# Kernel optimization log

Hardware: AMD Instinct MI355X
Metric: run time of the kernel (lower is better)

Reference implementation:

```python
import jax, jax.numpy as jnp
from jax import lax
import numpy as np

N_QUBITS = 8
Q_DEPTH = 10
DIM = 256  # 2**8

# basis-state bit table; wire 0 = most-significant bit (PennyLane convention)
_bits = ((np.arange(DIM)[:, None] >> (N_QUBITS - 1 - np.arange(N_QUBITS))) & 1)
# phase layer: S on even wires (phase i), T on odd wires (phase e^{i pi/4})
_ph = np.where(np.arange(N_QUBITS) % 2 == 0, 1j, np.exp(1j * np.pi / 4))
_diag = np.prod(np.power(_ph[None, :], _bits), axis=1)
# entangling_layer_3 CZ pattern
_cz = np.ones(DIM)
for i, j in [(0, 1), (2, 3), (4, 5), (6, 7), (1, 2), (3, 4), (5, 6)]:
    _cz = _cz * ((-1.0) ** (_bits[:, i] * _bits[:, j]))
DIAG = jnp.asarray((_diag * _cz).astype(np.complex64))  # phase+CZ layer fused diagonal
ZSIGNS = jnp.asarray((1 - 2 * _bits).astype(np.float32))  # [256, 8] PauliZ eigenvalues
H_GATE = jnp.asarray((np.array([[1.0, 1.0], [1.0, -1.0]]) / np.sqrt(2.0)).astype(np.complex64))
X_GATE = jnp.asarray(np.array([[0.0, 1.0], [1.0, 0.0]]).astype(np.complex64))
EYE2 = jnp.eye(2, dtype=jnp.complex64)
BN_EPS = 1e-5


def apply_1q(state, U, w):
    """Apply 2x2 gate U on wire w; state: [B, 2,2,...,2]."""
    state = jnp.moveaxis(state, w + 1, -1)
    state = jnp.matmul(state, U.T)
    return jnp.moveaxis(state, -1, w + 1)


def quantum_net(features, q_params):
    """Batched statevector sim of quantum_net_3. features [B,256], q_params [80] -> [B,8]."""
    f = features / jnp.linalg.norm(features, axis=1, keepdims=True)
    state = f.astype(jnp.complex64).reshape((-1,) + (2,) * N_QUBITS)
    for w in range(N_QUBITS):
        state = apply_1q(state, H_GATE, w)
    qw = q_params.reshape(Q_DEPTH, N_QUBITS)
    for layer in range(Q_DEPTH):
        for w in range(N_QUBITS):
            t = qw[layer, w]
            c = jnp.cos(t / 2).astype(jnp.complex64)
            s = jnp.sin(t / 2).astype(jnp.complex64)
            U = c * EYE2 + (-1j) * s * X_GATE  # RX(t)
            state = apply_1q(state, U, w)
        flat = state.reshape(-1, DIM) * DIAG  # phase layer + CZ entangling (diagonal)
        state = flat.reshape((-1,) + (2,) * N_QUBITS)
    sv = state.reshape(-1, DIM)
    probs = sv.real ** 2 + sv.imag ** 2
    return probs @ ZSIGNS  # [B, 8] expval(PauliZ_i)


def conv2d(x, w, b):
    y = lax.conv_general_dilated(x, w, (1, 1), 'SAME', dimension_numbers=('NCHW', 'OIHW', 'NCHW'))
    return y + b[None, :, None, None]


def bn(x, gamma, beta, mean, var):  # eval-mode BatchNorm2d
    inv = gamma / jnp.sqrt(var + BN_EPS)
    return x * inv[None, :, None, None] + (beta - mean * inv)[None, :, None, None]


def maxpool2(x):
    return lax.reduce_window(x, -jnp.inf, lax.max, (1, 1, 2, 2), (1, 1, 2, 2), 'VALID')


def setup_inputs() -> dict:
    key = jax.random.key(0)
    ks = jax.random.split(key, 16)
    B = 1024
    return {
        'x': jax.random.normal(ks[0], (B, 1, 28, 28), dtype=jnp.float32),
        'conv1_w': 0.1 * jax.random.normal(ks[1], (32, 1, 3, 3), dtype=jnp.float32),
        'conv1_b': jnp.zeros((32,), jnp.float32),
        'bn1_gamma': jnp.ones((32,), jnp.float32),
        'bn1_beta': jnp.zeros((32,), jnp.float32),
        'bn1_mean': jnp.zeros((32,), jnp.float32),
        'bn1_var': jnp.ones((32,), jnp.float32),
        'conv2_w': 0.05 * jax.random.normal(ks[2], (64, 32, 3, 3), dtype=jnp.float32),
        'conv2_b': jnp.zeros((64,), jnp.float32),
        'bn2_gamma': jnp.ones((64,), jnp.float32),
        'bn2_beta': jnp.zeros((64,), jnp.float32),
        'bn2_mean': jnp.zeros((64,), jnp.float32),
        'bn2_var': jnp.ones((64,), jnp.float32),
        'fc_w': 0.01 * jax.random.normal(ks[3], (256, 64 * 7 * 7), dtype=jnp.float32),
        'fc_b': jnp.zeros((256,), jnp.float32),
        'q_params': 0.1 * jax.random.normal(ks[4], (Q_DEPTH * N_QUBITS,), dtype=jnp.float32),
        'p1_w': 0.01 * jax.random.normal(ks[5], (128, 8), dtype=jnp.float32),
        'p1_b': jnp.zeros((128,), jnp.float32),
        'p2_w': 0.01 * jax.random.normal(ks[6], (64, 128), dtype=jnp.float32),
        'p2_b': jnp.zeros((64,), jnp.float32),
        'p3_w': 0.01 * jax.random.normal(ks[7], (10, 64), dtype=jnp.float32),
        'p3_b': jnp.zeros((10,), jnp.float32),
    }


def reference(x, conv1_w, conv1_b, bn1_gamma, bn1_beta, bn1_mean, bn1_var,
              conv2_w, conv2_b, bn2_gamma, bn2_beta, bn2_mean, bn2_var,
              fc_w, fc_b, q_params, p1_w, p1_b, p2_w, p2_b, p3_w, p3_b):
    h = maxpool2(jax.nn.relu(bn(conv2d(x, conv1_w, conv1_b), bn1_gamma, bn1_beta, bn1_mean, bn1_var)))
    h = maxpool2(jax.nn.relu(bn(conv2d(h, conv2_w, conv2_b), bn2_gamma, bn2_beta, bn2_mean, bn2_var)))
    h = h.reshape(h.shape[0], -1)  # [B, 64*7*7]
    feats = jnp.tanh(h @ fc_w.T + fc_b)  # [B, 256]
    q = quantum_net(feats, q_params)  # [B, 8]
    z = jax.nn.relu(q @ p1_w.T + p1_b)  # dropout = identity (eval)
    z = jax.nn.relu(z @ p2_w.T + p2_b)
    return z @ p3_w.T + p3_b
```

## Files before the change

### kernel.cpp

```cpp
#include <hip/hip_runtime.h>
#include <math.h>


#define B_SZ 1024

#define OFF_FCWP   0
#define OFF_W2F    802816
#define OFF_SC2    821600
#define OFF_SH2    821664
#define OFF_H1     821728
#define OFF_H2P    7244256

#define KSPLIT_FC 14
#define TS 40

typedef __attribute__((ext_vector_type(8))) short s16x8;
typedef __attribute__((ext_vector_type(4))) float f32x4;

__constant__ float C_COS8[8] = {1.f, 0.70710678f, 0.f, -0.70710678f, -1.f, -0.70710678f, 0.f, 0.70710678f};
__constant__ float C_SIN8[8] = {0.f, 0.70710678f, 1.f, 0.70710678f, 0.f, -0.70710678f, -1.f, -0.70710678f};

__device__ __forceinline__ unsigned short bf16_rne(float f) {
  unsigned u = __float_as_uint(f);
  unsigned r = u + 0x7FFFu + ((u >> 16) & 1u);
  return (unsigned short)(r >> 16);
}
__device__ __forceinline__ int div14(int m) {
  return __float2int_rz((float)m * 0.07142858f);
}

__global__ __launch_bounds__(256) void fused_front_kernel(
    const float* __restrict__ x, const float* __restrict__ c1w, const float* __restrict__ c1b,
    const float* __restrict__ bn1g, const float* __restrict__ bn1b, const float* __restrict__ bn1m,
    const float* __restrict__ bn1v,
    const float* __restrict__ c2w,
    const float* __restrict__ bn2g, const float* __restrict__ bn2b, const float* __restrict__ bn2m,
    const float* __restrict__ bn2v, const float* __restrict__ c2b,
    const float* __restrict__ fc_w,
    float* __restrict__ ws) {
  const int blk = blockIdx.x, tid = threadIdx.x;
  __shared__ float smem[3136];

  if (blk >= 1024) {
    if (blk < 1280) {
      const int n = blk - 1024;
      const float* src = fc_w + n * 3136;
      for (int i = tid; i < 3136; i += 256) smem[i] = src[i];
      __syncthreads();
      unsigned short* us = (unsigned short*)ws;
      const int nt = n >> 4, nl = n & 15;
      for (int idx = tid; idx < 784; idx += 256) {
        const int part = (idx >= 392);
        const int rest = idx - part * 392;
        const int kg = rest >> 2, q = rest & 3;
        s16x8 v;
#pragma unroll
        for (int j = 0; j < 8; ++j) {
          const int k = kg * 32 + q * 8 + j;
          float f = smem[(k & 63) * 49 + (k >> 6)];
          unsigned short hi = bf16_rne(f);
          unsigned short r = hi;
          if (part) r = bf16_rne(f - __uint_as_float((unsigned)hi << 16));
          v[j] = (short)r;
        }
        *(s16x8*)&us[((((kg * 16 + nt) * 2 + part)) << 9) + (q * 16 + nl) * 8] = v;
      }
    } else if (blk < 1424) {
      int g = (blk - 1280) * 256 + tid;
      int j = g & 7, L = (g >> 3) & 63, rest = g >> 9;
      int h = rest & 1; rest >>= 1;
      int t = rest % 9, w = rest / 9;
      int occ = w * 16 + (L & 15);
      int ic  = (L >> 4) * 8 + j;
      float v = c2w[occ * 288 + ic * 9 + t];
      unsigned short hi = bf16_rne(v);
      unsigned short res = hi;
      if (h) res = bf16_rne(v - __uint_as_float((unsigned)hi << 16));
      ((unsigned short*)(ws + OFF_W2F))[g] = res;
    } else {
      if (tid < 64) {
        float inv = bn2g[tid] / sqrtf(bn2v[tid] + 1e-5f);
        ws[OFF_SC2 + tid] = inv;
        ws[OFF_SH2 + tid] = c2b[tid] * inv + bn2b[tid] - bn2m[tid] * inv;
      }
    }
    return;
  }

  const int b = blk;
  float (*xs)[32] = (float (*)[32])smem;
  float* w1s  = smem + 960;
  float* sc1s = smem + 1248;
  float* sh1s = smem + 1280;
  float* h1 = ws + OFF_H1;

  if (tid < 240) ((float4*)smem)[tid] = make_float4(0.f, 0.f, 0.f, 0.f);
  __syncthreads();
  const float* xb = x + b * 784;
  for (int i = tid; i < 784; i += 256) {
    int y = i / 28, c = i - y * 28;
    xs[y + 1][c + 1] = xb[i];
  }
  for (int i = tid; i < 288; i += 256) w1s[i] = c1w[(i & 31) * 9 + (i >> 5)];
  if (tid < 32) {
    float inv = bn1g[tid] / sqrtf(bn1v[tid] + 1e-5f);
    sc1s[tid] = inv;
    sh1s[tid] = c1b[tid] * inv + bn1b[tid] - bn1m[tid] * inv;
  }
  __syncthreads();

  for (int t = tid; t < 448; t += 256) {
    const int oc = t & 31, py = t >> 5;
    float wv[9];
#pragma unroll
    for (int k = 0; k < 9; ++k) wv[k] = w1s[k * 32 + oc];
    float acc0[28], acc1[28];
#pragma unroll
    for (int j = 0; j < 28; ++j) { acc0[j] = 0.f; acc1[j] = 0.f; }
#pragma unroll
    for (int r = 0; r < 4; ++r) {
      const int pr = 2 * py + r;
      float row[32];
#pragma unroll
      for (int q = 0; q < 8; ++q) {
        float4 v = *(const float4*)&xs[pr][4 * q];
        row[4 * q] = v.x; row[4 * q + 1] = v.y; row[4 * q + 2] = v.z; row[4 * q + 3] = v.w;
      }
      if (r <= 2) {
#pragma unroll
        for (int kx = 0; kx < 3; ++kx) {
          const float w = wv[r * 3 + kx];
#pragma unroll
          for (int xx = 0; xx < 28; ++xx) acc0[xx] = fmaf(row[xx + kx], w, acc0[xx]);
        }
      }
      if (r >= 1) {
#pragma unroll
        for (int kx = 0; kx < 3; ++kx) {
          const float w = wv[(r - 1) * 3 + kx];
#pragma unroll
          for (int xx = 0; xx < 28; ++xx) acc1[xx] = fmaf(row[xx + kx], w, acc1[xx]);
        }
      }
    }
    const float sc = sc1s[oc], sh = sh1s[oc];
    float* dst = h1 + b * 6272 + oc * 196 + py * 14;
#pragma unroll
    for (int px = 0; px < 14; ++px) {
      float v0 = fmaxf(fmaf(acc0[2 * px], sc, sh), 0.f);
      float v1 = fmaxf(fmaf(acc0[2 * px + 1], sc, sh), 0.f);
      float v2 = fmaxf(fmaf(acc1[2 * px], sc, sh), 0.f);
      float v3 = fmaxf(fmaf(acc1[2 * px + 1], sc, sh), 0.f);
      dst[px] = fmaxf(fmaxf(v0, v1), fmaxf(v2, v3));
    }
  }
}

__global__ __launch_bounds__(256, 2) void conv2_kernel(
    const float* __restrict__ h1, const float* __restrict__ w2f_f,
    const float* __restrict__ sc2, const float* __restrict__ sh2,
    unsigned short* __restrict__ h2hi, unsigned short* __restrict__ h2lo) {
  const int b = blockIdx.x, tid = threadIdx.x;
  const int lane = tid & 63, w = tid >> 6;
  const int mh = w >> 1, nh = w & 1;

  __shared__ unsigned char lds_raw[50176];
  unsigned short* tile_hi = (unsigned short*)lds_raw;
  unsigned short* tile_lo = (unsigned short*)(lds_raw + 21760);
  float* conv_out = (float*)lds_raw;

  const unsigned short* w2f = (const unsigned short*)w2f_f;
  s16x8 bf[9][2][2];
#pragma unroll
  for (int t = 0; t < 9; ++t)
#pragma unroll
    for (int ntl = 0; ntl < 2; ++ntl)
#pragma unroll
      for (int h = 0; h < 2; ++h)
        bf[t][ntl][h] = *(const s16x8*)&w2f[(((((nh * 2 + ntl) * 9 + t) * 2 + h)) << 9) + lane * 8];

  {
    float4* z = (float4*)lds_raw;
    for (int i = tid; i < 2720; i += 256) z[i] = make_float4(0.f, 0.f, 0.f, 0.f);
  }
  __syncthreads();

  if (tid < 196) {
    const int y = div14(tid), x = tid - y * 14;
    const int sp = ((y + 1) * 16 + (x + 1)) * TS;
    const float* src = h1 + b * 6272 + tid;
#pragma unroll
    for (int c = 0; c < 4; ++c) {
      s16x8 hv, lv;
#pragma unroll
      for (int j = 0; j < 8; ++j) {
        float v = src[(c * 8 + j) * 196];
        unsigned short h16 = bf16_rne(v);
        hv[j] = (short)h16;
        lv[j] = (short)bf16_rne(v - __uint_as_float((unsigned)h16 << 16));
      }
      *(s16x8*)&tile_hi[sp + c * 8] = hv;
      *(s16x8*)&tile_lo[sp + c * 8] = lv;
    }
  }
  __syncthreads();

  const int nmt = 7 - mh;
  const int mt0 = mh * 7;
  f32x4 acc[7][2];
#pragma unroll
  for (int i = 0; i < 7; ++i) { acc[i][0] = (f32x4){0,0,0,0}; acc[i][1] = (f32x4){0,0,0,0}; }

  const int kg8 = (lane >> 4) * 8;
#pragma unroll
  for (int mi = 0; mi < 7; ++mi) {
    if (mi < nmt) {
      const int m = (mt0 + mi) * 16 + (lane & 15);
      const int y = div14(m), x = m - y * 14;
      const int base = (y * 16 + x) * TS + kg8;
#pragma unroll
      for (int dy = 0; dy < 3; ++dy) {
#pragma unroll
        for (int dx = 0; dx < 3; ++dx) {
          const int off = base + (dy * 16 + dx) * TS;
          s16x8 ah = *(s16x8*)&tile_hi[off];
          s16x8 al = *(s16x8*)&tile_lo[off];
          const int t = dy * 3 + dx;
#pragma unroll
          for (int ntl = 0; ntl < 2; ++ntl) {
            acc[mi][ntl] = __builtin_amdgcn_mfma_f32_16x16x32_bf16(ah, bf[t][ntl][0], acc[mi][ntl], 0, 0, 0);
            acc[mi][ntl] = __builtin_amdgcn_mfma_f32_16x16x32_bf16(ah, bf[t][ntl][1], acc[mi][ntl], 0, 0, 0);
            acc[mi][ntl] = __builtin_amdgcn_mfma_f32_16x16x32_bf16(al, bf[t][ntl][0], acc[mi][ntl], 0, 0, 0);
          }
        }
      }
    }
  }
  __syncthreads();

#pragma unroll
  for (int mi = 0; mi < 7; ++mi) {
    if (mi < nmt) {
#pragma unroll
      for (int ntl = 0; ntl < 2; ++ntl) {
        const int oc = nh * 32 + ntl * 16 + (lane & 15);
        const float sc = sc2[oc], sh = sh2[oc];
#pragma unroll
        for (int r = 0; r < 4; ++r) {
          const int m = (mt0 + mi) * 16 + (lane >> 4) * 4 + r;
          if (m < 196) conv_out[m * 64 + oc] = fmaxf(fmaf(acc[mi][ntl][r], sc, sh), 0.f);
        }
      }
    }
  }
  __syncthreads();

  const int oc = tid & 63;
#pragma unroll
  for (int i = 0; i < 13; ++i) {
    const int ps = i * 4 + (tid >> 6);
    if (ps < 49) {
      const int py = (ps * 37) >> 8, px = ps - py * 7;
      const int m00 = py * 28 + px * 2;
      float v0 = conv_out[m00 * 64 + oc];
      float v1 = conv_out[(m00 + 1) * 64 + oc];
      float v2 = conv_out[(m00 + 14) * 64 + oc];
      float v3 = conv_out[(m00 + 15) * 64 + oc];
      float vm = fmaxf(fmaxf(v0, v1), fmaxf(v2, v3));
      unsigned short hv = bf16_rne(vm);
      const int idx = b * 3136 + ps * 64 + oc;
      h2hi[idx] = hv;
      h2lo[idx] = bf16_rne(vm - __uint_as_float((unsigned)hv << 16));
    }
  }
}

__global__ __launch_bounds__(256) void fc_mfma_kernel(
    const unsigned short* __restrict__ h2hi, const unsigned short* __restrict__ h2lo,
    const unsigned short* __restrict__ Bfrag, float* __restrict__ Part) {
  const int tid = threadIdx.x;
  const int lane = tid & 63, w = tid >> 6;
  const int nt0 = blockIdx.x * 4, z = blockIdx.z;
  const int mrow = blockIdx.y * 64 + w * 16 + (lane & 15);
  const int kg8 = (lane >> 4) * 8;
  const unsigned short* arow_hi = h2hi + mrow * 3136 + kg8;
  const unsigned short* arow_lo = h2lo + mrow * 3136 + kg8;

  f32x4 acc[4];
#pragma unroll
  for (int i = 0; i < 4; ++i) acc[i] = (f32x4){0.f, 0.f, 0.f, 0.f};

#pragma unroll
  for (int c = 0; c < 7; ++c) {
    const int kg = z * 7 + c;
    s16x8 ah = *(const s16x8*)(arow_hi + kg * 32);
    s16x8 al = *(const s16x8*)(arow_lo + kg * 32);
#pragma unroll
    for (int nf = 0; nf < 4; ++nf) {
      const unsigned short* bp = Bfrag + (size_t)((kg * 16 + nt0 + nf) * 2) * 512 + lane * 8;
      s16x8 bh = *(const s16x8*)bp;
      s16x8 bl = *(const s16x8*)(bp + 512);
      acc[nf] = __builtin_amdgcn_mfma_f32_16x16x32_bf16(ah, bh, acc[nf], 0, 0, 0);
      acc[nf] = __builtin_amdgcn_mfma_f32_16x16x32_bf16(ah, bl, acc[nf], 0, 0, 0);
      acc[nf] = __builtin_amdgcn_mfma_f32_16x16x32_bf16(al, bh, acc[nf], 0, 0, 0);
    }
  }

  float* dst = Part + (size_t)z * 262144;
  const int mbase = blockIdx.y * 64 + w * 16 + (lane >> 4) * 4;
  const int nbase = (lane & 15);
#pragma unroll
  for (int nf = 0; nf < 4; ++nf) {
#pragma unroll
    for (int r = 0; r < 4; ++r) {
      dst[(mbase + r) * 256 + (nt0 + nf) * 16 + nbase] = acc[nf][r];
    }
  }
}

__global__ __launch_bounds__(64) void quantum_kernel(
    const float* __restrict__ Part, const float* __restrict__ fc_b,
    const float* __restrict__ qp,
    const float* __restrict__ p1w, const float* __restrict__ p1b,
    const float* __restrict__ p2w, const float* __restrict__ p2b,
    const float* __restrict__ p3w, const float* __restrict__ p3b,
    float* __restrict__ out) {
  const int b = blockIdx.x, lane = threadIdx.x;
  __shared__ float csl[160];

  for (int g = lane; g < 80; g += 64) {
    float t = 0.5f * qp[g];
    csl[2 * g] = cosf(t);
    csl[2 * g + 1] = sinf(t);
  }
  __syncthreads();

  float fa[4];
#pragma unroll
  for (int a = 0; a < 4; ++a) {
    const int idx = a * 64 + lane;
    float f = fc_b[idx];
#pragma unroll
    for (int z = 0; z < KSPLIT_FC; ++z) f += Part[z * 262144 + b * 256 + idx];
    fa[a] = tanhf(f);
  }
  float ss = fa[0] * fa[0] + fa[1] * fa[1] + fa[2] * fa[2] + fa[3] * fa[3];
#pragma unroll
  for (int off = 32; off >= 1; off >>= 1) ss += __shfl_xor(ss, off);
  const float inv = 1.0f / sqrtf(ss);

  float re[4], im[4];
#pragma unroll
  for (int a = 0; a < 4; ++a) { re[a] = fa[a] * inv; im[a] = 0.f; }

  float dre[4], dim_[4];
#pragma unroll
  for (int a = 0; a < 4; ++a) {
    const int i = a * 64 + lane;
    const int k8 = (2 * __popc(i & 0xAA) + __popc(i & 0x55)) & 7;
    float dr = C_COS8[k8], di = C_SIN8[k8];
    int par = ((i >> 7) & (i >> 6)) ^ ((i >> 5) & (i >> 4)) ^ ((i >> 3) & (i >> 2)) ^ ((i >> 1) & i)
            ^ ((i >> 6) & (i >> 5)) ^ ((i >> 4) & (i >> 3)) ^ ((i >> 2) & (i >> 1));
    if (par & 1) { dr = -dr; di = -di; }
    dre[a] = dr; dim_[a] = di;
  }

  const float RS = 0.70710678118654752f;

#define H_PAIR(u, v)                                        \
  { float tur = re[u], tui = im[u];                         \
    re[u] = (tur + re[v]) * RS; im[u] = (tui + im[v]) * RS; \
    re[v] = (tur - re[v]) * RS; im[v] = (tui - im[v]) * RS; }
  H_PAIR(0, 2) H_PAIR(1, 3)
  H_PAIR(0, 1) H_PAIR(2, 3)
#pragma unroll
  for (int w = 2; w < 8; ++w) {
    const int m = 1 << (7 - w);
    const float sgn = (lane & m) ? -1.f : 1.f;
#pragma unroll
    for (int a = 0; a < 4; ++a) {
      float pre = __shfl_xor(re[a], m);
      float pim = __shfl_xor(im[a], m);
      re[a] = fmaf(sgn, re[a], pre) * RS;
      im[a] = fmaf(sgn, im[a], pim) * RS;
    }
  }

#define RX_PAIR(u, v, c, s)                                   \
  { float ur = re[u], ui = im[u], wr = re[v], wi = im[v];     \
    re[u] = fmaf(s, wi, c * ur); im[u] = fmaf(-s, wr, c * ui);\
    re[v] = fmaf(s, ui, c * wr); im[v] = fmaf(-s, ur, c * wi); }
  for (int layer = 0; layer < 10; ++layer) {
    const float* cs = &csl[16 * layer];
    { const float c = cs[0], s = cs[1]; RX_PAIR(0, 2, c, s) RX_PAIR(1, 3, c, s) }
    { const float c = cs[2], s = cs[3]; RX_PAIR(0, 1, c, s) RX_PAIR(2, 3, c, s) }
#pragma unroll
    for (int w = 2; w < 8; ++w) {
      const int m = 1 << (7 - w);
      const float c = cs[2 * w], s = cs[2 * w + 1];
#pragma unroll
      for (int a = 0; a < 4; ++a) {
        float pre = __shfl_xor(re[a], m);
        float pim = __shfl_xor(im[a], m);
        float nre = fmaf(s, pim, c * re[a]);
        float nim = fmaf(-s, pre, c * im[a]);
        if (w == 7) {
          float tre = nre * dre[a] - nim * dim_[a];
          nim = fmaf(nre, dim_[a], nim * dre[a]);
          nre = tre;
        }
        re[a] = nre; im[a] = nim;
      }
    }
  }

  float prb[4];
#pragma unroll
  for (int a = 0; a < 4; ++a) prb[a] = re[a] * re[a] + im[a] * im[a];
  float qv[8];
#pragma unroll
  for (int w = 0; w < 8; ++w) {
    float v;
    if (w == 0)      v = prb[0] + prb[1] - prb[2] - prb[3];
    else if (w == 1) v = prb[0] - prb[1] + prb[2] - prb[3];
    else {
      const int m = 1 << (7 - w);
      const float sgn = (lane & m) ? -1.f : 1.f;
      v = sgn * (prb[0] + prb[1] + prb[2] + prb[3]);
    }
#pragma unroll
    for (int off = 32; off >= 1; off >>= 1) v += __shfl_xor(v, off);
    qv[w] = v;
  }

  float z1a = p1b[lane], z1b = p1b[lane + 64];
#pragma unroll
  for (int k = 0; k < 8; ++k) {
    z1a = fmaf(qv[k], p1w[lane * 8 + k], z1a);
    z1b = fmaf(qv[k], p1w[(lane + 64) * 8 + k], z1b);
  }
  z1a = fmaxf(z1a, 0.f); z1b = fmaxf(z1b, 0.f);

  float acc2 = p2b[lane];
  const float* row2 = p2w + lane * 128;
#pragma unroll
  for (int kc = 0; kc < 64; kc += 4) {
    float4 w0 = *(const float4*)&row2[kc];
    float4 w1 = *(const float4*)&row2[64 + kc];
    float wv0[4] = {w0.x, w0.y, w0.z, w0.w};
    float wv1[4] = {w1.x, w1.y, w1.z, w1.w};
#pragma unroll
    for (int j = 0; j < 4; ++j) {
      acc2 = fmaf(__shfl(z1a, kc + j), wv0[j], acc2);
      acc2 = fmaf(__shfl(z1b, kc + j), wv1[j], acc2);
    }
  }
  const float z2 = fmaxf(acc2, 0.f);

#pragma unroll
  for (int n = 0; n < 10; ++n) {
    float p = z2 * p3w[n * 64 + lane];
#pragma unroll
    for (int off = 32; off >= 1; off >>= 1) p += __shfl_xor(p, off);
    if (lane == n) out[b * 10 + n] = p + p3b[n];
  }
}

extern "C" void kernel_launch(void* const* d_in, const int* in_sizes, int n_in,
                              void* d_out, int out_size, void* d_ws, size_t ws_size,
                              hipStream_t stream) {
  (void)in_sizes; (void)n_in; (void)out_size; (void)ws_size;
  const float* x    = (const float*)d_in[0];
  const float* c1w  = (const float*)d_in[1];
  const float* c1b  = (const float*)d_in[2];
  const float* bn1g = (const float*)d_in[3];
  const float* bn1b = (const float*)d_in[4];
  const float* bn1m = (const float*)d_in[5];
  const float* bn1v = (const float*)d_in[6];
  const float* c2w  = (const float*)d_in[7];
  const float* c2b  = (const float*)d_in[8];
  const float* bn2g = (const float*)d_in[9];
  const float* bn2b = (const float*)d_in[10];
  const float* bn2m = (const float*)d_in[11];
  const float* bn2v = (const float*)d_in[12];
  const float* fc_w = (const float*)d_in[13];
  const float* fc_b = (const float*)d_in[14];
  const float* qp   = (const float*)d_in[15];
  const float* p1w  = (const float*)d_in[16];
  const float* p1b  = (const float*)d_in[17];
  const float* p2w  = (const float*)d_in[18];
  const float* p2b  = (const float*)d_in[19];
  const float* p3w  = (const float*)d_in[20];
  const float* p3b  = (const float*)d_in[21];
  float* ws = (float*)d_ws;
  float* outp = (float*)d_out;

  unsigned short* h2hi = (unsigned short*)(ws + OFF_H2P);
  unsigned short* h2lo = h2hi + 3211264;
  const unsigned short* bfrag = (const unsigned short*)ws;

  fused_front_kernel<<<1425, 256, 0, stream>>>(x, c1w, c1b, bn1g, bn1b, bn1m, bn1v,
                                               c2w, bn2g, bn2b, bn2m, bn2v, c2b, fc_w, ws);
  conv2_kernel<<<B_SZ, 256, 0, stream>>>(ws + OFF_H1, ws + OFF_W2F, ws + OFF_SC2, ws + OFF_SH2,
                                         h2hi, h2lo);
  fc_mfma_kernel<<<dim3(4, 16, KSPLIT_FC), 256, 0, stream>>>(h2hi, h2lo, bfrag, ws + OFF_H1);
  quantum_kernel<<<B_SZ, 64, 0, stream>>>(ws + OFF_H1, fc_b, qp, p1w, p1b, p2w, p2b, p3w, p3b, outp);
}
```

Baseline: 179.5 us.

## Fuse conv1 into conv2 kernel, writing pooled activations straight to LDS tiles

Conv1+BN+ReLU+maxpool now runs inside the conv2 block and writes its bf16 hi/lo split directly into the shared-memory input tiles. This removes the global round trip of the h1 intermediate (about 25 MB written and read back) and one kernel boundary. Weight packing moves to a separate small prep kernel that runs first. The cost is that the scalar conv1 phase now runs in a block using about 49KB of LDS and the register-resident weight fragments. That can lower occupancy for the conv1 part and serialise it before the MFMA work in the same block.

```diff
diff --git a/kernel.cpp b/kernel.cpp
--- a/kernel.cpp
+++ b/kernel.cpp
@@ -29,73 +29,93 @@
   return __float2int_rz((float)m * 0.07142858f);
 }
 
-__global__ __launch_bounds__(256) void fused_front_kernel(
+__global__ __launch_bounds__(256) void prep_pack_kernel(
+    const float* __restrict__ fc_w, const float* __restrict__ c2w,
+    const float* __restrict__ bn2g, const float* __restrict__ bn2b, const float* __restrict__ bn2m,
+    const float* __restrict__ bn2v, const float* __restrict__ c2b,
+    float* __restrict__ ws) {
+  const int blk = blockIdx.x, tid = threadIdx.x;
+  __shared__ float smem[3136];
+
+  if (blk < 256) {
+    const int n = blk;
+    const float* src = fc_w + n * 3136;
+    for (int i = tid; i < 3136; i += 256) smem[i] = src[i];
+    __syncthreads();
+    unsigned short* us = (unsigned short*)ws;
+    const int nt = n >> 4, nl = n & 15;
+    for (int idx = tid; idx < 784; idx += 256) {
+      const int part = (idx >= 392);
+      const int rest = idx - part * 392;
+      const int kg = rest >> 2, q = rest & 3;
+      s16x8 v;
+#pragma unroll
+      for (int j = 0; j < 8; ++j) {
+        const int k = kg * 32 + q * 8 + j;
+        float f = smem[(k & 63) * 49 + (k >> 6)];
+        unsigned short hi = bf16_rne(f);
+        unsigned short r = hi;
+        if (part) r = bf16_rne(f - __uint_as_float((unsigned)hi << 16));
+        v[j] = (short)r;
+      }
+      *(s16x8*)&us[((((kg * 16 + nt) * 2 + part)) << 9) + (q * 16 + nl) * 8] = v;
+    }
+  } else if (blk < 400) {
+    int g = (blk - 256) * 256 + tid;
+    int j = g & 7, L = (g >> 3) & 63, rest = g >> 9;
+    int h = rest & 1; rest >>= 1;
+    int t = rest % 9, w = rest / 9;
+    int occ = w * 16 + (L & 15);
+    int ic  = (L >> 4) * 8 + j;
+    float v = c2w[occ * 288 + ic * 9 + t];
+    unsigned short hi = bf16_rne(v);
+    unsigned short res = hi;
+    if (h) res = bf16_rne(v - __uint_as_float((unsigned)hi << 16));
+    ((unsigned short*)(ws + OFF_W2F))[g] = res;
+  } else {
+    if (tid < 64) {
+      float inv = bn2g[tid] / sqrtf(bn2v[tid] + 1e-5f);
+      ws[OFF_SC2 + tid] = inv;
+      ws[OFF_SH2 + tid] = c2b[tid] * inv + bn2b[tid] - bn2m[tid] * inv;
+    }
+  }
+}
+
+__global__ __launch_bounds__(256, 2) void conv_fused_kernel(
     const float* __restrict__ x, const float* __restrict__ c1w, const float* __restrict__ c1b,
     const float* __restrict__ bn1g, const float* __restrict__ bn1b, const float* __restrict__ bn1m,
     const float* __restrict__ bn1v,
-    const float* __restrict__ c2w,
-    const float* __restrict__ bn2g, const float* __restrict__ bn2b, const float* __restrict__ bn2m,
-    const float* __restrict__ bn2v, const float* __restrict__ c2b,
-    const float* __restrict__ fc_w,
-    float* __restrict__ ws) {
-  const int blk = blockIdx.x, tid = threadIdx.x;
-  __shared__ float smem[3136];
-
-  if (blk >= 1024) {
-    if (blk < 1280) {
-      const int n = blk - 1024;
-      const float* src = fc_w + n * 3136;
-      for (int i = tid; i < 3136; i += 256) smem[i] = src[i];
-      __syncthreads();
-      unsigned short* us = (unsigned short*)ws;
-      const int nt = n >> 4, nl = n & 15;
-      for (int idx = tid; idx < 784; idx += 256) {
-        const int part = (idx >= 392);
-        const int rest = idx - part * 392;
-        const int kg = rest >> 2, q = rest & 3;
-        s16x8 v;
-#pragma unroll
-        for (int j = 0; j < 8; ++j) {
-          const int k = kg * 32 + q * 8 + j;
-          float f = smem[(k & 63) * 49 + (k >> 6)];
-          unsigned short hi = bf16_rne(f);
-          unsigned short r = hi;
-          if (part) r = bf16_rne(f - __uint_as_float((unsigned)hi << 16));
-          v[j] = (short)r;
-        }
-        *(s16x8*)&us[((((kg * 16 + nt) * 2 + part)) << 9) + (q * 16 + nl) * 8] = v;
-      }
-    } else if (blk < 1424) {
-      int g = (blk - 1280) * 256 + tid;
-      int j = g & 7, L = (g >> 3) & 63, rest = g >> 9;
-      int h = rest & 1; rest >>= 1;
-      int t = rest % 9, w = rest / 9;
-      int occ = w * 16 + (L & 15);
-      int ic  = (L >> 4) * 8 + j;
-      float v = c2w[occ * 288 + ic * 9 + t];
-      unsigned short hi = bf16_rne(v);
-      unsigned short res = hi;
-      if (h) res = bf16_rne(v - __uint_as_float((unsigned)hi << 16));
-      ((unsigned short*)(ws + OFF_W2F))[g] = res;
-    } else {
-      if (tid < 64) {
-        float inv = bn2g[tid] / sqrtf(bn2v[tid] + 1e-5f);
-        ws[OFF_SC2 + tid] = inv;
-        ws[OFF_SH2 + tid] = c2b[tid] * inv + bn2b[tid] - bn2m[tid] * inv;
-      }
-    }
-    return;
-  }
-
-  const int b = blk;
-  float (*xs)[32] = (float (*)[32])smem;
-  float* w1s  = smem + 960;
-  float* sc1s = smem + 1248;
-  float* sh1s = smem + 1280;
-  float* h1 = ws + OFF_H1;
-
-  if (tid < 240) ((float4*)smem)[tid] = make_float4(0.f, 0.f, 0.f, 0.f);
-  __syncthreads();
+    const float* __restrict__ w2f_f, const float* __restrict__ sc2, const float* __restrict__ sh2,
+    unsigned short* __restrict__ h2hi, unsigned short* __restrict__ h2lo) {
+  const int b = blockIdx.x, tid = threadIdx.x;
+  const int lane = tid & 63, w = tid >> 6;
+  const int mh = w >> 1, nh = w & 1;
+
+  __shared__ unsigned char lds_raw[50176];
+  unsigned short* tile_hi = (unsigned short*)lds_raw;
+  unsigned short* tile_lo = (unsigned short*)(lds_raw + 21760);
+  float* conv_out = (float*)lds_raw;
+  float (*xs)[32] = (float (*)[32])(lds_raw + 43520);
+  float* w1s  = (float*)(lds_raw + 47360);
+  float* sc1s = (float*)(lds_raw + 48512);
+  float* sh1s = (float*)(lds_raw + 48640);
+
+  const unsigned short* w2f = (const unsigned short*)w2f_f;
+  s16x8 bf[9][2][2];
+#pragma unroll
+  for (int t = 0; t < 9; ++t)
+#pragma unroll
+    for (int ntl = 0; ntl < 2; ++ntl)
+#pragma unroll
+      for (int h = 0; h < 2; ++h)
+        bf[t][ntl][h] = *(const s16x8*)&w2f[(((((nh * 2 + ntl) * 9 + t) * 2 + h)) << 9) + lane * 8];
+
+  {
+    float4* z = (float4*)lds_raw;
+    for (int i = tid; i < 2960; i += 256) z[i] = make_float4(0.f, 0.f, 0.f, 0.f);
+  }
+  __syncthreads();
+
   const float* xb = x + b * 784;
   for (int i = tid; i < 784; i += 256) {
     int y = i / 28, c = i - y * 28;
@@ -129,78 +149,32 @@
       if (r <= 2) {
 #pragma unroll
         for (int kx = 0; kx < 3; ++kx) {
-          const float w = wv[r * 3 + kx];
-#pragma unroll
-          for (int xx = 0; xx < 28; ++xx) acc0[xx] = fmaf(row[xx + kx], w, acc0[xx]);
+          const float ww = wv[r * 3 + kx];
+#pragma unroll
+          for (int xx = 0; xx < 28; ++xx) acc0[xx] = fmaf(row[xx + kx], ww, acc0[xx]);
         }
       }
       if (r >= 1) {
 #pragma unroll
         for (int kx = 0; kx < 3; ++kx) {
-          const float w = wv[(r - 1) * 3 + kx];
-#pragma unroll
-          for (int xx = 0; xx < 28; ++xx) acc1[xx] = fmaf(row[xx + kx], w, acc1[xx]);
+          const float ww = wv[(r - 1) * 3 + kx];
+#pragma unroll
+          for (int xx = 0; xx < 28; ++xx) acc1[xx] = fmaf(row[xx + kx], ww, acc1[xx]);
         }
       }
     }
     const float sc = sc1s[oc], sh = sh1s[oc];
-    float* dst = h1 + b * 6272 + oc * 196 + py * 14;
 #pragma unroll
     for (int px = 0; px < 14; ++px) {
       float v0 = fmaxf(fmaf(acc0[2 * px], sc, sh), 0.f);
       float v1 = fmaxf(fmaf(acc0[2 * px + 1], sc, sh), 0.f);
       float v2 = fmaxf(fmaf(acc1[2 * px], sc, sh), 0.f);
       float v3 = fmaxf(fmaf(acc1[2 * px + 1], sc, sh), 0.f);
-      dst[px] = fmaxf(fmaxf(v0, v1), fmaxf(v2, v3));
-    }
-  }
-}
-
-__global__ __launch_bounds__(256, 2) void conv2_kernel(
-    const float* __restrict__ h1, const float* __restrict__ w2f_f,
-    const float* __restrict__ sc2, const float* __restrict__ sh2,
-    unsigned short* __restrict__ h2hi, unsigned short* __restrict__ h2lo) {
-  const int b = blockIdx.x, tid = threadIdx.x;
-  const int lane = tid & 63, w = tid >> 6;
-  const int mh = w >> 1, nh = w & 1;
-
-  __shared__ unsigned char lds_raw[50176];
-  unsigned short* tile_hi = (unsigned short*)lds_raw;
-  unsigned short* tile_lo = (unsigned short*)(lds_raw + 21760);
-  float* conv_out = (float*)lds_raw;
-
-  const unsigned short* w2f = (const unsigned short*)w2f_f;
-  s16x8 bf[9][2][2];
-#pragma unroll
-  for (int t = 0; t < 9; ++t)
-#pragma unroll
-    for (int ntl = 0; ntl < 2; ++ntl)
-#pragma unroll
-      for (int h = 0; h < 2; ++h)
-        bf[t][ntl][h] = *(const s16x8*)&w2f[(((((nh * 2 + ntl) * 9 + t) * 2 + h)) << 9) + lane * 8];
-
-  {
-    float4* z = (float4*)lds_raw;
-    for (int i = tid; i < 2720; i += 256) z[i] = make_float4(0.f, 0.f, 0.f, 0.f);
-  }
-  __syncthreads();
-
-  if (tid < 196) {
-    const int y = div14(tid), x = tid - y * 14;
-    const int sp = ((y + 1) * 16 + (x + 1)) * TS;
-    const float* src = h1 + b * 6272 + tid;
-#pragma unroll
-    for (int c = 0; c < 4; ++c) {
-      s16x8 hv, lv;
-#pragma unroll
-      for (int j = 0; j < 8; ++j) {
-        float v = src[(c * 8 + j) * 196];
-        unsigned short h16 = bf16_rne(v);
-        hv[j] = (short)h16;
-        lv[j] = (short)bf16_rne(v - __uint_as_float((unsigned)h16 << 16));
-      }
-      *(s16x8*)&tile_hi[sp + c * 8] = hv;
-      *(s16x8*)&tile_lo[sp + c * 8] = lv;
+      float vm = fmaxf(fmaxf(v0, v1), fmaxf(v2, v3));
+      unsigned short hv = bf16_rne(vm);
+      const int sp = ((py + 1) * 16 + (px + 1)) * TS + oc;
+      tile_hi[sp] = hv;
+      tile_lo[sp] = bf16_rne(vm - __uint_as_float((unsigned)hv << 16));
     }
   }
   __syncthreads();
@@ -216,8 +190,8 @@
   for (int mi = 0; mi < 7; ++mi) {
     if (mi < nmt) {
       const int m = (mt0 + mi) * 16 + (lane & 15);
-      const int y = div14(m), x = m - y * 14;
-      const int base = (y * 16 + x) * TS + kg8;
+      const int y = div14(m), xx_ = m - y * 14;
+      const int base = (y * 16 + xx_) * TS + kg8;
 #pragma unroll
       for (int dy = 0; dy < 3; ++dy) {
 #pragma unroll
@@ -499,10 +473,10 @@
   unsigned short* h2lo = h2hi + 3211264;
   const unsigned short* bfrag = (const unsigned short*)ws;
 
-  fused_front_kernel<<<1425, 256, 0, stream>>>(x, c1w, c1b, bn1g, bn1b, bn1m, bn1v,
-                                               c2w, bn2g, bn2b, bn2m, bn2v, c2b, fc_w, ws);
-  conv2_kernel<<<B_SZ, 256, 0, stream>>>(ws + OFF_H1, ws + OFF_W2F, ws + OFF_SC2, ws + OFF_SH2,
-                                         h2hi, h2lo);
+  prep_pack_kernel<<<401, 256, 0, stream>>>(fc_w, c2w, bn2g, bn2b, bn2m, bn2v, c2b, ws);
+  conv_fused_kernel<<<B_SZ, 256, 0, stream>>>(x, c1w, c1b, bn1g, bn1b, bn1m, bn1v,
+                                              ws + OFF_W2F, ws + OFF_SC2, ws + OFF_SH2,
+                                              h2hi, h2lo);
   fc_mfma_kernel<<<dim3(4, 16, KSPLIT_FC), 256, 0, stream>>>(h2hi, h2lo, bfrag, ws + OFF_H1);
   quantum_kernel<<<B_SZ, 64, 0, stream>>>(ws + OFF_H1, fc_b, qp, p1w, p1b, p2w, p2b, p3w, p3b, outp);
 }
```

New measurement: 179.2 us. About the same (-0.1%).
